# Kernel optimization log

Measured on AMD Instinct MI355X. Metric: run time of the kernel, lower is better.

Reference implementation:

```python
import jax, jax.numpy as jnp
import numpy as np

HEADS = 16
DIM_HEAD = 64
QUERY_DIM = 1024
INNER = HEADS * DIM_HEAD  # 1024
SCALE = DIM_HEAD ** -0.5
B, T = 4, 2048


def setup_inputs() -> dict:
    key = jax.random.key(0)
    ks = jax.random.split(key, 7)
    s = 0.02
    return {
        "hidden_states": jax.random.normal(ks[0], (B, T, QUERY_DIM), dtype=jnp.float32),
        "attention_mask": jax.random.randint(ks[1], (B, T), 0, 2, dtype=jnp.int32),
        "Wq": jax.random.normal(ks[2], (QUERY_DIM, INNER), dtype=jnp.float32) * s,
        "Wk": jax.random.normal(ks[3], (QUERY_DIM, INNER), dtype=jnp.float32) * s,
        "Wv": jax.random.normal(ks[4], (QUERY_DIM, INNER), dtype=jnp.float32) * s,
        "Wo": jax.random.normal(ks[5], (INNER, QUERY_DIM), dtype=jnp.float32) * s,
        "bo": jnp.zeros((QUERY_DIM,), dtype=jnp.float32),
    }


def reference(hidden_states, attention_mask, Wq, Wk, Wv, Wo, bo):
    # QKV projections (bias=False)
    q = hidden_states @ Wq  # [B,T,INNER]
    k = hidden_states @ Wk
    v = hidden_states @ Wv
    # split heads: b t (h d) -> b h t d
    def split(x):
        b, t, _ = x.shape
        return x.reshape(b, t, HEADS, DIM_HEAD).transpose(0, 2, 1, 3)
    q, k, v = split(q), split(k), split(v)
    sim = jnp.einsum('bhid,bhjd->bhij', q, k) * SCALE  # [B,H,T,T]
    neg = jnp.finfo(sim.dtype).min
    mask = attention_mask[:, None, None, :]  # [B,1,1,T]
    sim = jnp.where(mask == 0, neg, sim)
    attn = jax.nn.softmax(sim, axis=-1)
    out = jnp.einsum('bhij,bhjd->bhid', attn, v)  # [B,H,T,D]
    out = out.transpose(0, 2, 1, 3).reshape(hidden_states.shape[0], hidden_states.shape[1], INNER)
    return out @ Wo + bo  # dropout p=0.0 -> identity
```

## Files before the change

### kernel.cpp

```cpp
#include <hip/hip_runtime.h>
#include <stdint.h>

typedef __attribute__((ext_vector_type(8))) __bf16 bf16x8;
typedef __attribute__((ext_vector_type(4))) float f32x4;
typedef __attribute__((ext_vector_type(16))) float f32x16;

#define QSCALE 0.18033688011112042f

static __device__ __forceinline__ unsigned short f2bf(float x) {
  return __builtin_bit_cast(unsigned short, (__bf16)x);
}
static __device__ __forceinline__ unsigned pkbf(float a, float b) {
  union { unsigned short h[2]; unsigned u; } r;
  r.h[0] = f2bf(a); r.h[1] = f2bf(b); return r.u;
}
static __device__ __forceinline__ void async16(const void* g, void* l) {
  __builtin_amdgcn_global_load_lds(
      (const __attribute__((address_space(1))) void*)g,
      (__attribute__((address_space(3))) void*)l, 16, 0, 0);
}

__global__ __launch_bounds__(256) void k_prep(const float* __restrict__ hs,
                                              const float* __restrict__ Wq,
                                              const float* __restrict__ Wk,
                                              const float* __restrict__ Wv,
                                              const float* __restrict__ Wo,
                                              unsigned short* __restrict__ hs_bf,
                                              unsigned short* __restrict__ wt_qkv,
                                              unsigned short* __restrict__ wot) {
  __shared__ float tile[64][65];
  const int bid = blockIdx.x;
  if (bid < 8192) {
    const int i = bid * 256 + threadIdx.x;
    float4 v = ((const float4*)hs)[i];
    ushort4 o;
    o.x = f2bf(v.x); o.y = f2bf(v.y); o.z = f2bf(v.z); o.w = f2bf(v.w);
    ((ushort4*)hs_bf)[i] = o;
    return;
  }
  const int idx = bid - 8192;
  const int mat = idx >> 8;
  const float* W = (mat == 0) ? Wq : (mat == 1) ? Wk : (mat == 2) ? Wv : Wo;
  const float scale = (mat == 0) ? QSCALE : 1.0f;
  const int n0 = (idx & 15) * 64, k0 = ((idx >> 4) & 15) * 64;
  const int t = threadIdx.x, c = t & 63;
#pragma unroll
  for (int j = 0; j < 16; ++j) {
    int r = j * 4 + (t >> 6);
    tile[r][c] = W[(size_t)(k0 + r) * 1024 + n0 + c] * scale;
  }
  __syncthreads();
  unsigned short* dst = (mat < 3) ? (wt_qkv + (size_t)mat * 1024 * 1024) : wot;
#pragma unroll
  for (int j = 0; j < 16; ++j) {
    int nr = j * 4 + (t >> 6);
    dst[(size_t)(n0 + nr) * 1024 + k0 + c] = f2bf(tile[c][nr]);
  }
}

__global__ __launch_bounds__(256) void k_gemm_qkv(const unsigned short* __restrict__ A,
                                                  const unsigned short* __restrict__ Bt,
                                                  unsigned short* __restrict__ q_lin,
                                                  unsigned short* __restrict__ k_lin,
                                                  unsigned short* __restrict__ vT) {
  __shared__ __align__(16) unsigned short aT[2][128 * 32];
  __shared__ __align__(16) unsigned short bT[2][128 * 32];
  const int tid = threadIdx.x, lane = tid & 63, w = tid >> 6;
  const int wr = w >> 1, wc = w & 1;
  int flat = blockIdx.y * 24 + blockIdx.x;
  flat = (flat & 7) * 192 + (flat >> 3);
  const int m0 = (flat / 24) * 128, n0 = (flat % 24) * 128;
  const char* Ab = (const char*)A;
  const char* Bb = (const char*)Bt;
  char* aTb = (char*)aT; char* bTb = (char*)bT;
  f32x4 acc[4][4] = {};

  const int ci0 = w * 2, bo0 = ci0 * 1024 + lane * 16;
  const int srow0 = bo0 >> 6, scol0 = bo0 & 63;
#define G_STAGE(buf, kt)                                                              \
  {                                                                                   \
    _Pragma("unroll")                                                                 \
    for (int j = 0; j < 2; ++j) {                                                     \
      const int row = srow0 + j * 16;                                                 \
      async16(Ab + ((size_t)(m0 + row) * 1024 + (kt) * 32) * 2 + scol0,               \
              aTb + (buf) * 8192 + (ci0 + j) * 1024);                                 \
      async16(Bb + ((size_t)(n0 + row) * 1024 + (kt) * 32) * 2 + scol0,               \
              bTb + (buf) * 8192 + (ci0 + j) * 1024);                                 \
    }                                                                                 \
  }

  G_STAGE(0, 0);
  __syncthreads();
  for (int kt = 0; kt < 32; ++kt) {
    const int cur = kt & 1;
    if (kt + 1 < 32) G_STAGE(cur ^ 1, kt + 1);
    bf16x8 af[4], bfr[4];
#pragma unroll
    for (int mi = 0; mi < 4; ++mi)
      af[mi] = *(const bf16x8*)(aTb + cur * 8192 +
               ((wr * 64 + mi * 16 + (lane & 15)) * 32 + (lane >> 4) * 8) * 2);
#pragma unroll
    for (int ni = 0; ni < 4; ++ni)
      bfr[ni] = *(const bf16x8*)(bTb + cur * 8192 +
               ((wc * 64 + ni * 16 + (lane & 15)) * 32 + (lane >> 4) * 8) * 2);
#pragma unroll
    for (int mi = 0; mi < 4; ++mi)
#pragma unroll
      for (int ni = 0; ni < 4; ++ni)
        acc[mi][ni] = __builtin_amdgcn_mfma_f32_16x16x32_bf16(af[mi], bfr[ni], acc[mi][ni], 0, 0, 0);
    __syncthreads();
  }
#undef G_STAGE

  const int mat = n0 >> 10;
  const int nn0 = n0 & 1023;
  if (mat < 2) {
    unsigned short* dst = (mat == 0) ? q_lin : k_lin;
#pragma unroll
    for (int mi = 0; mi < 4; ++mi) {
      const int r0 = m0 + wr * 64 + mi * 16 + (lane >> 4) * 4;
#pragma unroll
      for (int ni = 0; ni < 4; ++ni) {
        const int c = nn0 + wc * 64 + ni * 16 + (lane & 15);
#pragma unroll
        for (int r = 0; r < 4; ++r)
          dst[(size_t)(r0 + r) * 1024 + c] = f2bf(acc[mi][ni][r]);
      }
    }
  } else {
#pragma unroll
    for (int mi = 0; mi < 4; ++mi) {
      const int r0 = m0 + wr * 64 + mi * 16 + (lane >> 4) * 4;
      const int b = r0 >> 11, tt = r0 & 2047;
#pragma unroll
      for (int ni = 0; ni < 4; ++ni) {
        const int c = nn0 + wc * 64 + ni * 16 + (lane & 15);
        const int h = c >> 6, d = c & 63;
        ushort4 o;
        o.x = f2bf(acc[mi][ni][0]); o.y = f2bf(acc[mi][ni][1]);
        o.z = f2bf(acc[mi][ni][2]); o.w = f2bf(acc[mi][ni][3]);
        *(ushort4*)(vT + ((size_t)((b * 16 + h) * 64 + d) << 11) + tt) = o;
      }
    }
  }
}

__global__ __launch_bounds__(256, 3) void k_attn(const unsigned short* __restrict__ q_lin,
                                                 const unsigned short* __restrict__ k_lin,
                                                 const unsigned short* __restrict__ vT,
                                                 const int* __restrict__ mask,
                                                 unsigned short* __restrict__ o_lin) {
  __shared__ __align__(16) unsigned short Kt[2][64 * 64];
  __shared__ __align__(16) unsigned short Vt[2][64 * 64];
  __shared__ __align__(16) unsigned short Pl[4][32 * 64];
  __shared__ __align__(16) float biasl[2][64];
  const int tid = threadIdx.x, lane = tid & 63, w = tid >> 6;
  const int qi = lane & 31, hi = lane >> 5;
  int flat = blockIdx.y * 16 + blockIdx.x;
  flat = (flat & 7) * 128 + (flat >> 3);
  const int bh = flat >> 4, b = bh >> 4, h = bh & 15;
  const int t0 = (flat & 15) * 128;
  const unsigned short* qbp = q_lin + (size_t)b * 2048 * 1024 + h * 64;
  const unsigned short* kbp = k_lin + (size_t)b * 2048 * 1024 + h * 64;
  const unsigned short* vbp = vT + ((size_t)bh * 64 << 11);
  unsigned short* obp = o_lin + (size_t)b * 2048 * 1024 + h * 64;
  const int* mp = mask + b * 2048;
  char* KtB = (char*)Kt; char* VtB = (char*)Vt;
  char* PlB = (char*)(&Pl[w][0]);
  const int rsw = (qi & 7) << 4;

  bf16x8 qf[4];
  {
    const unsigned short* qrow = qbp + (size_t)(t0 + w * 32 + qi) * 1024;
#pragma unroll
    for (int s = 0; s < 4; ++s)
      qf[s] = *(const bf16x8*)(qrow + s * 16 + hi * 8);
  }

  f32x16 oaccA = {}, oaccB = {};
  float m_ = -3.0e38f, l_ = 0.f;

  const int sci = w * 2, sbo = sci * 1024 + lane * 16;
  const int srow = sbo >> 7;
  const int scolb = (sbo & 127) ^ ((srow & 7) << 4);
#define A_STAGE(buf, kv0)                                                             \
  {                                                                                   \
    _Pragma("unroll")                                                                 \
    for (int j = 0; j < 2; ++j) {                                                     \
      const int row = srow + j * 8;                                                   \
      async16(kbp + (size_t)((kv0) + row) * 1024 + (scolb >> 1),                      \
              KtB + (buf) * 8192 + (sci + j) * 1024);                                 \
      async16(vbp + (size_t)row * 2048 + (kv0) + (scolb >> 1),                        \
              VtB + (buf) * 8192 + (sci + j) * 1024);                                 \
    }                                                                                 \
    if (tid < 64) biasl[buf][tid] = (mp[(kv0) + tid] == 0) ? -__builtin_inff() : 0.0f;\
  }

  A_STAGE(0, 0);
  __syncthreads();

  for (int kt = 0; kt < 32; ++kt) {
    const int cur = kt & 1;
    if (kt + 1 < 32) A_STAGE(cur ^ 1, (kt + 1) * 64);

    f32x16 sA = {}, sB = {};
    __builtin_amdgcn_s_setprio(1);
#pragma unroll
    for (int s = 0; s < 4; ++s) {
      bf16x8 kf = *(const bf16x8*)(KtB + cur * 8192 + (qi)*128 + ((s * 32 + hi * 16) ^ rsw));
      sA = __builtin_amdgcn_mfma_f32_32x32x16_bf16(kf, qf[s], sA, 0, 0, 0);
    }
#pragma unroll
    for (int s = 0; s < 4; ++s) {
      bf16x8 kf = *(const bf16x8*)(KtB + cur * 8192 + (32 + qi) * 128 + ((s * 32 + hi * 16) ^ rsw));
      sB = __builtin_amdgcn_mfma_f32_32x32x16_bf16(kf, qf[s], sB, 0, 0, 0);
    }
    __builtin_amdgcn_s_setprio(0);

    float e[32];
#pragma unroll
    for (int u = 0; u < 4; ++u) {
      const float4 b4 = ((const float4*)biasl[cur])[2 * u + hi];
      e[4 * u + 0] = sA[4 * u + 0] + b4.x; e[4 * u + 1] = sA[4 * u + 1] + b4.y;
      e[4 * u + 2] = sA[4 * u + 2] + b4.z; e[4 * u + 3] = sA[4 * u + 3] + b4.w;
    }
#pragma unroll
    for (int u = 0; u < 4; ++u) {
      const float4 b4 = ((const float4*)biasl[cur])[8 + 2 * u + hi];
      e[16 + 4 * u + 0] = sB[4 * u + 0] + b4.x; e[16 + 4 * u + 1] = sB[4 * u + 1] + b4.y;
      e[16 + 4 * u + 2] = sB[4 * u + 2] + b4.z; e[16 + 4 * u + 3] = sB[4 * u + 3] + b4.w;
    }

    float t16[16];
#pragma unroll
    for (int i = 0; i < 16; ++i) t16[i] = fmaxf(e[i], e[16 + i]);
#pragma unroll
    for (int i = 0; i < 8; ++i) t16[i] = fmaxf(t16[i], t16[8 + i]);
#pragma unroll
    for (int i = 0; i < 4; ++i) t16[i] = fmaxf(t16[i], t16[4 + i]);
    float mt = fmaxf(fmaxf(t16[0], t16[1]), fmaxf(t16[2], t16[3]));
    mt = fmaxf(mt, __shfl_xor(mt, 32));

    if (__any(mt > m_ + 8.0f)) {
      const float mn = fmaxf(m_, mt);
      const float sf = __builtin_amdgcn_exp2f(m_ - mn);
      m_ = mn; l_ *= sf;
#pragma unroll
      for (int r = 0; r < 16; ++r) { oaccA[r] *= sf; oaccB[r] *= sf; }
    }

#pragma unroll
    for (int i = 0; i < 32; ++i) e[i] = __builtin_amdgcn_exp2f(e[i] - m_);
    float u16[16];
#pragma unroll
    for (int i = 0; i < 16; ++i) u16[i] = e[i] + e[16 + i];
#pragma unroll
    for (int i = 0; i < 8; ++i) u16[i] += u16[8 + i];
#pragma unroll
    for (int i = 0; i < 4; ++i) u16[i] += u16[4 + i];
    float rs = (u16[0] + u16[1]) + (u16[2] + u16[3]);
    l_ += rs + __shfl_xor(rs, 32);

#pragma unroll
    for (int u = 0; u < 8; ++u) {
      uint2 pk;
      pk.x = pkbf(e[4 * u + 0], e[4 * u + 1]);
      pk.y = pkbf(e[4 * u + 2], e[4 * u + 3]);
      *(uint2*)(PlB + qi * 128 + ((16 * u + 8 * hi) ^ rsw)) = pk;
    }
    bf16x8 pw[4];
#pragma unroll
    for (int t = 0; t < 4; ++t)
      pw[t] = *(const bf16x8*)(PlB + qi * 128 + ((32 * t + 16 * hi) ^ rsw));

    __builtin_amdgcn_s_setprio(1);
#pragma unroll
    for (int t = 0; t < 4; ++t) {
      bf16x8 vf = *(const bf16x8*)(VtB + cur * 8192 + (qi)*128 + ((t * 32 + hi * 16) ^ rsw));
      oaccA = __builtin_amdgcn_mfma_f32_32x32x16_bf16(vf, pw[t], oaccA, 0, 0, 0);
    }
#pragma unroll
    for (int t = 0; t < 4; ++t) {
      bf16x8 vf = *(const bf16x8*)(VtB + cur * 8192 + (32 + qi) * 128 + ((t * 32 + hi * 16) ^ rsw));
      oaccB = __builtin_amdgcn_mfma_f32_32x32x16_bf16(vf, pw[t], oaccB, 0, 0, 0);
    }
    __builtin_amdgcn_s_setprio(0);
    __syncthreads();
  }
#undef A_STAGE

  const float inv = 1.0f / l_;
  unsigned short* orow = obp + (size_t)(t0 + w * 32 + qi) * 1024;
#pragma unroll
  for (int u = 0; u < 4; ++u) {
    ushort4 oa, ob;
    oa.x = f2bf(oaccA[4 * u + 0] * inv); oa.y = f2bf(oaccA[4 * u + 1] * inv);
    oa.z = f2bf(oaccA[4 * u + 2] * inv); oa.w = f2bf(oaccA[4 * u + 3] * inv);
    ob.x = f2bf(oaccB[4 * u + 0] * inv); ob.y = f2bf(oaccB[4 * u + 1] * inv);
    ob.z = f2bf(oaccB[4 * u + 2] * inv); ob.w = f2bf(oaccB[4 * u + 3] * inv);
    *(ushort4*)(orow + 8 * u + 4 * hi) = oa;
    *(ushort4*)(orow + 32 + 8 * u + 4 * hi) = ob;
  }
}

__global__ __launch_bounds__(256) void k_gemm_out(const unsigned short* __restrict__ A,
                                                  const unsigned short* __restrict__ Bt,
                                                  const float* __restrict__ bias,
                                                  float* __restrict__ out) {
  __shared__ __align__(16) unsigned short aT[2][128 * 32];
  __shared__ __align__(16) unsigned short bT[2][128 * 32];
  const int tid = threadIdx.x, lane = tid & 63, w = tid >> 6;
  const int wr = w >> 1, wc = w & 1;
  int flat = blockIdx.y * 8 + blockIdx.x;
  flat = (flat & 7) * 64 + (flat >> 3);
  const int m0 = (flat >> 3) * 128, n0 = (flat & 7) * 128;
  const char* Ab = (const char*)A;
  const char* Bb = (const char*)Bt;
  char* aTb = (char*)aT; char* bTb = (char*)bT;
  f32x4 acc[4][4] = {};

  const int ci0 = w * 2, bo0 = ci0 * 1024 + lane * 16;
  const int srow0 = bo0 >> 6, scol0 = bo0 & 63;
#define G_STAGE(buf, kt)                                                              \
  {                                                                                   \
    _Pragma("unroll")                                                                 \
    for (int j = 0; j < 2; ++j) {                                                     \
      const int row = srow0 + j * 16;                                                 \
      async16(Ab + ((size_t)(m0 + row) * 1024 + (kt) * 32) * 2 + scol0,               \
              aTb + (buf) * 8192 + (ci0 + j) * 1024);                                 \
      async16(Bb + ((size_t)(n0 + row) * 1024 + (kt) * 32) * 2 + scol0,               \
              bTb + (buf) * 8192 + (ci0 + j) * 1024);                                 \
    }                                                                                 \
  }

  G_STAGE(0, 0);
  __syncthreads();
  for (int kt = 0; kt < 32; ++kt) {
    const int cur = kt & 1;
    if (kt + 1 < 32) G_STAGE(cur ^ 1, kt + 1);
    bf16x8 af[4], bfr[4];
#pragma unroll
    for (int mi = 0; mi < 4; ++mi)
      af[mi] = *(const bf16x8*)(aTb + cur * 8192 +
               ((wr * 64 + mi * 16 + (lane & 15)) * 32 + (lane >> 4) * 8) * 2);
#pragma unroll
    for (int ni = 0; ni < 4; ++ni)
      bfr[ni] = *(const bf16x8*)(bTb + cur * 8192 +
               ((wc * 64 + ni * 16 + (lane & 15)) * 32 + (lane >> 4) * 8) * 2);
#pragma unroll
    for (int mi = 0; mi < 4; ++mi)
#pragma unroll
      for (int ni = 0; ni < 4; ++ni)
        acc[mi][ni] = __builtin_amdgcn_mfma_f32_16x16x32_bf16(af[mi], bfr[ni], acc[mi][ni], 0, 0, 0);
    __syncthreads();
  }
#undef G_STAGE
#pragma unroll
  for (int mi = 0; mi < 4; ++mi) {
    const int r0 = m0 + wr * 64 + mi * 16 + (lane >> 4) * 4;
#pragma unroll
    for (int ni = 0; ni < 4; ++ni) {
      const int c = n0 + wc * 64 + ni * 16 + (lane & 15);
      const float bb = bias[c];
#pragma unroll
      for (int r = 0; r < 4; ++r)
        out[(size_t)(r0 + r) * 1024 + c] = acc[mi][ni][r] + bb;
    }
  }
}

extern "C" void kernel_launch(void* const* d_in, const int* in_sizes, int n_in,
                              void* d_out, int out_size, void* d_ws, size_t ws_size,
                              hipStream_t stream) {
  const float* hs   = (const float*)d_in[0];
  const int*   mask = (const int*)d_in[1];
  const float* Wq   = (const float*)d_in[2];
  const float* Wk   = (const float*)d_in[3];
  const float* Wv   = (const float*)d_in[4];
  const float* Wo   = (const float*)d_in[5];
  const float* bo   = (const float*)d_in[6];
  float* out = (float*)d_out;

  const size_t MB = 1024 * 1024;
  char* ws = (char*)d_ws;
  unsigned short* hs_bf  = (unsigned short*)(ws);
  unsigned short* wt_qkv = (unsigned short*)(ws + 16 * MB);
  unsigned short* wot    = (unsigned short*)(ws + 22 * MB);
  unsigned short* q_lin  = (unsigned short*)(ws + 24 * MB);
  unsigned short* k_lin  = (unsigned short*)(ws + 40 * MB);
  unsigned short* vT     = (unsigned short*)(ws + 56 * MB);
  unsigned short* o_lin  = (unsigned short*)(ws + 72 * MB);

  k_prep<<<9216, 256, 0, stream>>>(hs, Wq, Wk, Wv, Wo, hs_bf, wt_qkv, wot);
  k_gemm_qkv<<<dim3(24, 64), 256, 0, stream>>>(hs_bf, wt_qkv, q_lin, k_lin, vT);
  k_attn<<<dim3(16, 64), 256, 0, stream>>>(q_lin, k_lin, vT, mask, o_lin);
  k_gemm_out<<<dim3(8, 64), 256, 0, stream>>>(o_lin, wot, bo, out);
}
```

Measured before the change: 315.9 us.

## Pass P between lanes by shuffle instead of LDS; precompute mask bias

The attention kernel no longer stages the bf16 probability tile through a per-wave LDS buffer. The P-to-B-operand transposition is now done with cross-half-wave shuffles, which frees 16KB of LDS. Launch bounds rise from 3 to 4 blocks per CU to use that room. The mask-to-additive-bias conversion moves into the prep kernel and is staged into LDS asynchronously alongside K/V, replacing the per-tile integer compare. The higher occupancy target may force register spills.

```diff
diff --git a/kernel.cpp b/kernel.cpp
--- a/kernel.cpp
+++ b/kernel.cpp
@@ -4,6 +4,7 @@
 typedef __attribute__((ext_vector_type(8))) __bf16 bf16x8;
 typedef __attribute__((ext_vector_type(4))) float f32x4;
 typedef __attribute__((ext_vector_type(16))) float f32x16;
+typedef __attribute__((ext_vector_type(4))) unsigned u32x4;
 
 #define QSCALE 0.18033688011112042f
 
@@ -25,9 +26,11 @@
                                               const float* __restrict__ Wk,
                                               const float* __restrict__ Wv,
                                               const float* __restrict__ Wo,
+                                              const int* __restrict__ mask,
                                               unsigned short* __restrict__ hs_bf,
                                               unsigned short* __restrict__ wt_qkv,
-                                              unsigned short* __restrict__ wot) {
+                                              unsigned short* __restrict__ wot,
+                                              float* __restrict__ bias_all) {
   __shared__ float tile[64][65];
   const int bid = blockIdx.x;
   if (bid < 8192) {
@@ -36,6 +39,15 @@
     ushort4 o;
     o.x = f2bf(v.x); o.y = f2bf(v.y); o.z = f2bf(v.z); o.w = f2bf(v.w);
     ((ushort4*)hs_bf)[i] = o;
+    return;
+  }
+  if (bid >= 9216) {
+    const int b = bid - 9216;
+#pragma unroll
+    for (int j = 0; j < 8; ++j) {
+      const int t = j * 256 + threadIdx.x;
+      bias_all[b * 2048 + t] = (mask[b * 2048 + t] == 0) ? -__builtin_inff() : 0.0f;
+    }
     return;
   }
   const int idx = bid - 8192;
@@ -145,14 +157,13 @@
   }
 }
 
-__global__ __launch_bounds__(256, 3) void k_attn(const unsigned short* __restrict__ q_lin,
+__global__ __launch_bounds__(256, 4) void k_attn(const unsigned short* __restrict__ q_lin,
                                                  const unsigned short* __restrict__ k_lin,
                                                  const unsigned short* __restrict__ vT,
-                                                 const int* __restrict__ mask,
+                                                 const float* __restrict__ bias_all,
                                                  unsigned short* __restrict__ o_lin) {
   __shared__ __align__(16) unsigned short Kt[2][64 * 64];
   __shared__ __align__(16) unsigned short Vt[2][64 * 64];
-  __shared__ __align__(16) unsigned short Pl[4][32 * 64];
   __shared__ __align__(16) float biasl[2][64];
   const int tid = threadIdx.x, lane = tid & 63, w = tid >> 6;
   const int qi = lane & 31, hi = lane >> 5;
@@ -164,9 +175,9 @@
   const unsigned short* kbp = k_lin + (size_t)b * 2048 * 1024 + h * 64;
   const unsigned short* vbp = vT + ((size_t)bh * 64 << 11);
   unsigned short* obp = o_lin + (size_t)b * 2048 * 1024 + h * 64;
-  const int* mp = mask + b * 2048;
+  const char* bbp = (const char*)(bias_all + b * 2048);
   char* KtB = (char*)Kt; char* VtB = (char*)Vt;
-  char* PlB = (char*)(&Pl[w][0]);
+  char* blB = (char*)biasl;
   const int rsw = (qi & 7) << 4;
 
   bf16x8 qf[4];
@@ -193,7 +204,8 @@
       async16(vbp + (size_t)row * 2048 + (kv0) + (scolb >> 1),                        \
               VtB + (buf) * 8192 + (sci + j) * 1024);                                 \
     }                                                                                 \
-    if (tid < 64) biasl[buf][tid] = (mp[(kv0) + tid] == 0) ? -__builtin_inff() : 0.0f;\
+    if (lane < 16) async16(bbp + (size_t)(kv0) * 4 + lane * 16,                       \
+                           blB + (buf) * 256 + lane * 16);                            \
   }
 
   A_STAGE(0, 0);
@@ -261,17 +273,30 @@
     float rs = (u16[0] + u16[1]) + (u16[2] + u16[3]);
     l_ += rs + __shfl_xor(rs, 32);
 
-#pragma unroll
-    for (int u = 0; u < 8; ++u) {
-      uint2 pk;
-      pk.x = pkbf(e[4 * u + 0], e[4 * u + 1]);
-      pk.y = pkbf(e[4 * u + 2], e[4 * u + 3]);
-      *(uint2*)(PlB + qi * 128 + ((16 * u + 8 * hi) ^ rsw)) = pk;
-    }
+    unsigned d[16];
+#pragma unroll
+    for (int j = 0; j < 8; ++j) {
+      d[2 * j] = pkbf(e[4 * j + 0], e[4 * j + 1]);
+      d[2 * j + 1] = pkbf(e[4 * j + 2], e[4 * j + 3]);
+    }
+    unsigned rcv[8];
+#pragma unroll
+    for (int t = 0; t < 4; ++t)
+#pragma unroll
+      for (int s = 0; s < 2; ++s) {
+        const unsigned snd = hi ? d[4 * t + s] : d[4 * t + 2 + s];
+        rcv[2 * t + s] = __shfl_xor(snd, 32);
+      }
     bf16x8 pw[4];
 #pragma unroll
-    for (int t = 0; t < 4; ++t)
-      pw[t] = *(const bf16x8*)(PlB + qi * 128 + ((32 * t + 16 * hi) ^ rsw));
+    for (int t = 0; t < 4; ++t) {
+      u32x4 u4;
+      u4.x = hi ? rcv[2 * t + 0] : d[4 * t + 0];
+      u4.y = hi ? rcv[2 * t + 1] : d[4 * t + 1];
+      u4.z = hi ? d[4 * t + 2] : rcv[2 * t + 0];
+      u4.w = hi ? d[4 * t + 3] : rcv[2 * t + 1];
+      pw[t] = __builtin_bit_cast(bf16x8, u4);
+    }
 
     __builtin_amdgcn_s_setprio(1);
 #pragma unroll
@@ -390,9 +415,10 @@
   unsigned short* k_lin  = (unsigned short*)(ws + 40 * MB);
   unsigned short* vT     = (unsigned short*)(ws + 56 * MB);
   unsigned short* o_lin  = (unsigned short*)(ws + 72 * MB);
-
-  k_prep<<<9216, 256, 0, stream>>>(hs, Wq, Wk, Wv, Wo, hs_bf, wt_qkv, wot);
+  float*          bias_a = (float*)(ws + 88 * MB);
+
+  k_prep<<<9220, 256, 0, stream>>>(hs, Wq, Wk, Wv, Wo, mask, hs_bf, wt_qkv, wot, bias_a);
   k_gemm_qkv<<<dim3(24, 64), 256, 0, stream>>>(hs_bf, wt_qkv, q_lin, k_lin, vT);
-  k_attn<<<dim3(16, 64), 256, 0, stream>>>(q_lin, k_lin, vT, mask, o_lin);
+  k_attn<<<dim3(16, 64), 256, 0, stream>>>(q_lin, k_lin, vT, bias_a, o_lin);
   k_gemm_out<<<dim3(8, 64), 256, 0, stream>>>(o_lin, wot, bo, out);
 }
```

New measurement: 312.2 us. Within noise of the previous version (-1.2%).
